# Performance work log

Hardware: AMD Instinct MI355X
Metric: run time of the kernel (lower is better)

## Reference

```python
import jax, jax.numpy as jnp
import numpy as np

DIM = 512
HEADS = 8
HEAD_DIM = DIM // HEADS
WINDOW = 128
TOKEN_SELF_ATTN_VALUE = -5e4  # lucidrains local-attention constant for shared_qk self mask


def setup_inputs() -> dict:
    key = jax.random.key(0)
    k1, k2, k3, k4 = jax.random.split(key, 4)
    B, N = 4, 8192
    x = jax.random.normal(k1, (B, N, DIM), dtype=jnp.float32)
    w_qkv = jax.random.normal(k2, (3 * DIM, DIM), dtype=jnp.float32) * (DIM ** -0.5)
    w_proj = jax.random.normal(k3, (DIM, DIM), dtype=jnp.float32) * (DIM ** -0.5)
    b_proj = jax.random.normal(k4, (DIM,), dtype=jnp.float32) * 0.01
    return {"x": x, "w_qkv": w_qkv, "w_proj": w_proj, "b_proj": b_proj}


def _look_around(b):
    # b: [B,H,nw,w,D] -> [B,H,nw,2w,D] = concat(prev_window, cur_window); window 0 padded with zeros
    padded = jnp.pad(b, ((0, 0), (0, 0), (1, 0), (0, 0), (0, 0)))
    return jnp.concatenate([padded[:, :, :-1], b], axis=3)


def _local_attn(q, k, v):
    # causal sliding-window attention, window=128, look_backward=1, shared_qk
    B, H, N, D = q.shape
    w = WINDOW
    nw = N // w
    scale = D ** -0.5
    # shared_qk: l2-normalize keys (F.normalize, eps=1e-12)
    k = k / jnp.clip(jnp.linalg.norm(k, axis=-1, keepdims=True), 1e-12, None)

    bq = q.reshape(B, H, nw, w, D)
    bk = _look_around(k.reshape(B, H, nw, w, D))  # [B,H,nw,2w,D]
    bv = _look_around(v.reshape(B, H, nw, w, D))

    t = jnp.arange(N).reshape(nw, w)
    t_pad = jnp.pad(t, ((1, 0), (0, 0)), constant_values=-1)
    bq_t = t                                         # [nw, w]
    bq_k = jnp.concatenate([t_pad[:-1], t], axis=1)  # [nw, 2w]

    sim = jnp.einsum('bhwie,bhwje->bhwij', bq, bk) * scale  # [B,H,nw,w,2w]

    self_mask = bq_t[:, :, None] == bq_k[:, None, :]
    causal_mask = bq_t[:, :, None] < bq_k[:, None, :]
    pad_mask = (bq_k == -1)[:, None, :]
    mask_value = -jnp.finfo(sim.dtype).max
    sim = jnp.where(self_mask, TOKEN_SELF_ATTN_VALUE, sim)
    sim = jnp.where(causal_mask | pad_mask, mask_value, sim)

    attn = jax.nn.softmax(sim, axis=-1)  # dropout is identity in eval mode
    out = jnp.einsum('bhwij,bhwje->bhwie', attn, bv)
    return out.reshape(B, H, N, D)


def reference(x, w_qkv, w_proj, b_proj):
    B, N, C = x.shape
    qkv = x @ w_qkv.T  # [B,N,3C]
    q, k, v = jnp.split(qkv, 3, axis=-1)
    to_heads = lambda t: t.reshape(B, N, HEADS, HEAD_DIM).transpose(0, 2, 1, 3)
    out = _local_attn(to_heads(q), to_heads(k), to_heads(v))  # [B,H,N,D]
    out = out.transpose(0, 2, 1, 3).reshape(B, N, C)
    return out @ w_proj.T + b_proj
```

## Files before the change

kernel.cpp:

```cpp
#include <hip/hip_runtime.h>
#include <stdint.h>

typedef uint16_t u16;
typedef __bf16 bf16x8 __attribute__((ext_vector_type(8)));
typedef float f32x4 __attribute__((ext_vector_type(4)));
typedef uint16_t u16x4 __attribute__((ext_vector_type(4)));
typedef uint16_t u16x8 __attribute__((ext_vector_type(8)));

typedef __attribute__((address_space(1))) void as1_void;
typedef __attribute__((address_space(3))) void as3_void;

__device__ __forceinline__ float bf2f(u16 b) {
    union { uint32_t u; float f; } v; v.u = ((uint32_t)b) << 16; return v.f;
}
__device__ __forceinline__ u16 f2bf(float f) {
    union { float f; uint32_t u; } v; v.f = f;
    uint32_t u = v.u;
    u += 0x7fffu + ((u >> 16) & 1u);
    return (u16)(u >> 16);
}
__device__ __forceinline__ void gload_lds16(const u16* g, u16* l) {
    __builtin_amdgcn_global_load_lds((as1_void*)g, (as3_void*)l, 16, 0, 0);
}

__global__ __launch_bounds__(256) void cvt3(
    const float* __restrict__ x,  u16* __restrict__ xb,
    const float* __restrict__ wq, u16* __restrict__ wqb,
    const float* __restrict__ wp, u16* __restrict__ wpb)
{
    const float* src; u16* dst; int base, nb;
    const int b = blockIdx.x;
    if (b < 1024)      { src = x;  dst = xb;  base = b;        nb = 1024; }
    else if (b < 1072) { src = wq; dst = wqb; base = b - 1024; nb = 48;   }
    else               { src = wp; dst = wpb; base = b - 1072; nb = 16;   }
    size_t i = ((size_t)base * 256 + threadIdx.x) * 8;
    const size_t stride = (size_t)nb * 256 * 8;
    #pragma unroll
    for (int it = 0; it < 8; ++it, i += stride) {
        f32x4 a = *(const f32x4*)(src + i);
        f32x4 c = *(const f32x4*)(src + i + 4);
        u16x8 o;
        o[0] = f2bf(a[0]); o[1] = f2bf(a[1]); o[2] = f2bf(a[2]); o[3] = f2bf(a[3]);
        o[4] = f2bf(c[0]); o[5] = f2bf(c[1]); o[6] = f2bf(c[2]); o[7] = f2bf(c[3]);
        *(u16x8*)(dst + i) = o;
    }
}

template<int NT, bool C_F32, bool NORMK, bool BIAS>
__global__ __launch_bounds__(512, 2) void gemm_pipe256(
    const u16* __restrict__ A, int lda,
    const u16* __restrict__ B, int ldb,
    const float* __restrict__ bias,
    void* __restrict__ Cv, int ldc)
{
    __shared__ u16 lA[4][256 * 32];
    __shared__ u16 lB[4][256 * 32];

    const int tid  = threadIdx.x;
    const int lane = tid & 63;
    const int wave = tid >> 6;
    const int wm = wave >> 2;
    const int wn = wave & 3;
    const int cl = lane & 15;
    const int gr = lane >> 4;

    int fid = blockIdx.y * gridDim.x + blockIdx.x;
    const int nwg = gridDim.x * gridDim.y;
    fid = (fid & 7) * (nwg >> 3) + (fid >> 3);
    const int row0 = (fid / gridDim.x) * 256;
    const int col0 = (fid % gridDim.x) * 256;

    f32x4 acc[8][4] = {};

    auto STAGE = [&](int t, int d) {
        const int k0 = t * 32;
        #pragma unroll
        for (int i = 0; i < 2; ++i) {
            const int id  = i * 512 + tid;
            const int row = id >> 2;
            const int sch = ((id & 3) - ((row >> 1) & 3)) & 3;
            gload_lds16(A + (size_t)(row0 + row) * lda + k0 + sch * 8, &lA[d][id * 8]);
            gload_lds16(B + (size_t)(col0 + row) * ldb + k0 + sch * 8, &lB[d][id * 8]);
        }
    };

    bf16x8 af[8], bfv[4];
    auto READ_A = [&](int t, int m) -> bf16x8 {
        const u16* la = lA[t & 3];
        const int ra = wm * 128 + m * 16 + cl;
        return *(const bf16x8*)&la[ra * 32 + ((gr + (ra >> 1)) & 3) * 8];
    };
    auto READ_B = [&](int t, int n) -> bf16x8 {
        const u16* lb = lB[t & 3];
        const int rb = wn * 64 + n * 16 + cl;
        return *(const bf16x8*)&lb[rb * 32 + ((gr + (rb >> 1)) & 3) * 8];
    };

    STAGE(0, 0); STAGE(1, 1); STAGE(2, 2);
    asm volatile("s_waitcnt vmcnt(4)" ::: "memory");
    __builtin_amdgcn_s_barrier();
    #pragma unroll
    for (int m = 0; m < 8; ++m) af[m] = READ_A(0, m);
    #pragma unroll
    for (int n = 0; n < 4; ++n) bfv[n] = READ_B(0, n);

    #pragma unroll
    for (int t = 0; t < NT; ++t) {
        if (t + 3 < NT) STAGE(t + 3, (t + 3) & 3);
        __builtin_amdgcn_s_setprio(1);
        #pragma unroll
        for (int m = 0; m < 8; ++m) {
            #pragma unroll
            for (int n = 0; n < 4; ++n)
                acc[m][n] = __builtin_amdgcn_mfma_f32_16x16x32_bf16(af[m], bfv[n], acc[m][n], 0, 0, 0);
            if (t + 1 < NT) af[m] = READ_A(t + 1, m);
        }
        __builtin_amdgcn_s_setprio(0);
        if (t + 1 < NT) {
            #pragma unroll
            for (int n = 0; n < 4; ++n) bfv[n] = READ_B(t + 1, n);
        }
        if (t < NT - 1) {
            asm volatile("s_waitcnt lgkmcnt(0)" ::: "memory");
            if (t + 3 < NT) asm volatile("s_waitcnt vmcnt(4)" ::: "memory");
            else            asm volatile("s_waitcnt vmcnt(0)" ::: "memory");
            __builtin_amdgcn_s_barrier();
        }
    }

    if constexpr (NORMK) {
        if (col0 + wn * 64 >= 512 && col0 + wn * 64 < 1024) {
            #pragma unroll
            for (int m = 0; m < 8; ++m)
                #pragma unroll
                for (int j = 0; j < 4; ++j) {
                    float ss = 0.f;
                    #pragma unroll
                    for (int n = 0; n < 4; ++n) ss += acc[m][n][j] * acc[m][n][j];
                    ss += __shfl_xor(ss, 1);
                    ss += __shfl_xor(ss, 2);
                    ss += __shfl_xor(ss, 4);
                    ss += __shfl_xor(ss, 8);
                    const float scl = 1.f / fmaxf(sqrtf(ss), 1e-12f);
                    #pragma unroll
                    for (int n = 0; n < 4; ++n) acc[m][n][j] *= scl;
                }
        }
    }

    #pragma unroll
    for (int m = 0; m < 8; ++m) {
        const int r = row0 + wm * 128 + m * 16 + gr * 4;
        #pragma unroll
        for (int n = 0; n < 4; ++n) {
            const int c = col0 + wn * 64 + n * 16 + cl;
            float bv = 0.f;
            if constexpr (BIAS) bv = bias[c];
            #pragma unroll
            for (int j = 0; j < 4; ++j) {
                const float val = acc[m][n][j] + bv;
                if constexpr (C_F32) ((float*)Cv)[(size_t)(r + j) * ldc + c] = val;
                else                 ((u16*)Cv)[(size_t)(r + j) * ldc + c] = f2bf(val);
            }
        }
    }
}

template<bool A_F32, bool C_F32, bool NORMK>
__global__ __launch_bounds__(256) void gemm_bt_f32(
    const void* __restrict__ Av, int lda,
    const float* __restrict__ B, int ldb,
    const float* __restrict__ bias,
    void* __restrict__ Cv, int ldc,
    int K)
{
    __shared__ u16 lA[128 * 32];
    __shared__ u16 lB[128 * 32];

    const int tid  = threadIdx.x;
    const int lane = tid & 63;
    const int wave = tid >> 6;
    const int wr   = (wave >> 1) * 64;
    const int wc   = (wave & 1) * 64;
    const int row0 = blockIdx.y * 128;
    const int col0 = blockIdx.x * 128;

    f32x4 acc[4][4] = {};

    for (int k0 = 0; k0 < K; k0 += 32) {
        #pragma unroll
        for (int i = 0; i < 4; ++i) {
            const int idx = i * 256 + tid;
            const int r = idx >> 3;
            const int p = (idx & 7) * 4;
            u16x4 a4, b4;
            if constexpr (A_F32) {
                const float* Af = (const float*)Av;
                f32x4 va = *(const f32x4*)(Af + (size_t)(row0 + r) * lda + k0 + p);
                a4[0] = f2bf(va[0]); a4[1] = f2bf(va[1]); a4[2] = f2bf(va[2]); a4[3] = f2bf(va[3]);
            } else {
                const u16* Ab = (const u16*)Av;
                a4 = *(const u16x4*)(Ab + (size_t)(row0 + r) * lda + k0 + p);
            }
            {
                f32x4 vb = *(const f32x4*)(B + (size_t)(col0 + r) * ldb + k0 + p);
                b4[0] = f2bf(vb[0]); b4[1] = f2bf(vb[1]); b4[2] = f2bf(vb[2]); b4[3] = f2bf(vb[3]);
            }
            *(u16x4*)&lA[r * 32 + p] = a4;
            *(u16x4*)&lB[r * 32 + p] = b4;
        }
        __syncthreads();

        bf16x8 af[4], bfv[4];
        #pragma unroll
        for (int m = 0; m < 4; ++m)
            af[m] = *(const bf16x8*)(lA + (wr + m * 16 + (lane & 15)) * 32 + (lane >> 4) * 8);
        #pragma unroll
        for (int n = 0; n < 4; ++n)
            bfv[n] = *(const bf16x8*)(lB + (wc + n * 16 + (lane & 15)) * 32 + (lane >> 4) * 8);
        #pragma unroll
        for (int m = 0; m < 4; ++m)
            #pragma unroll
            for (int n = 0; n < 4; ++n)
                acc[m][n] = __builtin_amdgcn_mfma_f32_16x16x32_bf16(af[m], bfv[n], acc[m][n], 0, 0, 0);
        __syncthreads();
    }

    if constexpr (NORMK) {
        if (col0 >= 512 && col0 < 1024) {
            #pragma unroll
            for (int m = 0; m < 4; ++m)
                #pragma unroll
                for (int j = 0; j < 4; ++j) {
                    float ss = 0.f;
                    #pragma unroll
                    for (int n = 0; n < 4; ++n) ss += acc[m][n][j] * acc[m][n][j];
                    ss += __shfl_xor(ss, 1);
                    ss += __shfl_xor(ss, 2);
                    ss += __shfl_xor(ss, 4);
                    ss += __shfl_xor(ss, 8);
                    const float scl = 1.f / fmaxf(sqrtf(ss), 1e-12f);
                    #pragma unroll
                    for (int n = 0; n < 4; ++n) acc[m][n][j] *= scl;
                }
        }
    }

    #pragma unroll
    for (int m = 0; m < 4; ++m) {
        const int r = row0 + wr + m * 16 + ((lane >> 4) << 2);
        #pragma unroll
        for (int n = 0; n < 4; ++n) {
            const int c = col0 + wc + n * 16 + (lane & 15);
            const float bv = bias ? bias[c] : 0.f;
            #pragma unroll
            for (int j = 0; j < 4; ++j) {
                const float val = acc[m][n][j] + bv;
                if constexpr (C_F32) ((float*)Cv)[(size_t)(r + j) * ldc + c] = val;
                else                 ((u16*)Cv)[(size_t)(r + j) * ldc + c] = f2bf(val);
            }
        }
    }
}

__global__ __launch_bounds__(512, 4) void attn_kernel(const u16* qkv, u16* o)
{
    constexpr int CC = 1536;
    constexpr int NTOK = 8192;
    constexpr int KP = 72;
    constexpr int VP = 136;
    constexpr int PP = 136;
    __shared__ u16 kn[128 * KP];
    __shared__ u16 vT[64 * VP];
    __shared__ u16 Pl[128 * PP];

    const int tid  = threadIdx.x;
    const int lane = tid & 63;
    const int wave = tid >> 6;
    const int cl = lane & 15;
    const int gr = lane >> 4;

    int blk = blockIdx.x;
    blk = (blk & 7) * (gridDim.x >> 3) + (blk >> 3);

    const int iw  = blk & 63;
    const int h   = (blk >> 6) & 7;
    const int b   = blk >> 9;

    const int tq0 = iw * 128;
    const int tkc0 = tq0 - 128;
    const int tkc1 = tq0;
    const size_t rowbase = (size_t)b * NTOK;
    const u16* qbase = qkv + rowbase * CC + h * 64;
    const u16* kbase = qbase + 512;
    const u16* vbase = qbase + 1024;

    const int wrow = wave * 16;
    bf16x8 qf[2];
    #pragma unroll
    for (int kk = 0; kk < 2; ++kk)
        qf[kk] = *(const bf16x8*)(qbase + (size_t)(tq0 + wrow + cl) * CC + kk * 32 + gr * 8);

    f32x4 oacc[4] = {};
    float m_run[4] = {-3.0e38f, -3.0e38f, -3.0e38f, -3.0e38f};
    float l_run[4] = {0.f, 0.f, 0.f, 0.f};

    auto CHUNK = [&](int tkc) {
        f32x4 s[8] = {};
        #pragma unroll
        for (int n = 0; n < 8; ++n)
            #pragma unroll
            for (int kk = 0; kk < 2; ++kk) {
                const bf16x8 kf = *(const bf16x8*)&kn[(n * 16 + cl) * KP + kk * 32 + gr * 8];
                s[n] = __builtin_amdgcn_mfma_f32_16x16x32_bf16(qf[kk], kf, s[n], 0, 0, 0);
            }
        float pmax[4] = {-3.0e38f, -3.0e38f, -3.0e38f, -3.0e38f};
        #pragma unroll
        for (int n = 0; n < 8; ++n) {
            const int tkk = tkc + n * 16 + cl;
            const bool pad = tkk < 0;
            #pragma unroll
            for (int j = 0; j < 4; ++j) {
                const int tq = tq0 + wrow + gr * 4 + j;
                float sv = s[n][j] * 0.125f;
                const int rel = tkk - tq;
                sv = (rel == 0) ? -5.0e4f : sv;
                sv = (rel > 0 || pad) ? -6.0e4f : sv;
                s[n][j] = sv;
                pmax[j] = fmaxf(pmax[j], sv);
            }
        }
        float cold[4];
        #pragma unroll
        for (int j = 0; j < 4; ++j) {
            pmax[j] = fmaxf(pmax[j], __shfl_xor(pmax[j], 1));
            pmax[j] = fmaxf(pmax[j], __shfl_xor(pmax[j], 2));
            pmax[j] = fmaxf(pmax[j], __shfl_xor(pmax[j], 4));
            pmax[j] = fmaxf(pmax[j], __shfl_xor(pmax[j], 8));
            const float mn = fmaxf(m_run[j], pmax[j]);
            cold[j] = __expf(m_run[j] - mn);
            m_run[j] = mn;
            l_run[j] *= cold[j];
        }
        #pragma unroll
        for (int n = 0; n < 8; ++n)
            #pragma unroll
            for (int j = 0; j < 4; ++j) {
                const float p = __expf(s[n][j] - m_run[j]);
                s[n][j] = p;
                l_run[j] += p;
            }
        #pragma unroll
        for (int n = 0; n < 4; ++n) {
            f32x4 t = oacc[n];
            t[0] *= cold[0]; t[1] *= cold[1]; t[2] *= cold[2]; t[3] *= cold[3];
            oacc[n] = t;
        }
        #pragma unroll
        for (int n = 0; n < 8; ++n)
            #pragma unroll
            for (int j = 0; j < 4; ++j)
                Pl[(wrow + gr * 4 + j) * PP + n * 16 + cl] = f2bf(s[n][j]);
        __syncthreads();
        #pragma unroll
        for (int kk = 0; kk < 4; ++kk) {
            const bf16x8 pa = *(const bf16x8*)&Pl[(wrow + cl) * PP + kk * 32 + gr * 8];
            #pragma unroll
            for (int n = 0; n < 4; ++n) {
                const bf16x8 vb = *(const bf16x8*)&vT[(n * 16 + cl) * VP + kk * 32 + gr * 8];
                oacc[n] = __builtin_amdgcn_mfma_f32_16x16x32_bf16(pa, vb, oacc[n], 0, 0, 0);
            }
        }
    };

    #pragma unroll
    for (int p = 0; p < 2; ++p) {
        const int id = tid + p * 512;
        const int row = id >> 3, dc = id & 7;
        u16x8 v8 = {};
        if (tkc0 >= 0) v8 = *(const u16x8*)(kbase + (size_t)(tkc0 + row) * CC + dc * 8);
        *(u16x8*)&kn[row * KP + dc * 8] = v8;
    }
    #pragma unroll
    for (int p = 0; p < 2; ++p) {
        const int id = tid + p * 512;
        const int key = id & 127, dc = id >> 7;
        u16x8 v8 = {};
        if (tkc0 >= 0) v8 = *(const u16x8*)(vbase + (size_t)(tkc0 + key) * CC + dc * 8);
        #pragma unroll
        for (int e = 0; e < 8; ++e) vT[(dc * 8 + e) * VP + key] = v8[e];
    }
    u16x8 kr[2], vr[2];
    #pragma unroll
    for (int p = 0; p < 2; ++p) {
        const int id = tid + p * 512;
        kr[p] = *(const u16x8*)(kbase + (size_t)(tkc1 + (id >> 3)) * CC + (id & 7) * 8);
        vr[p] = *(const u16x8*)(vbase + (size_t)(tkc1 + (id & 127)) * CC + (id >> 7) * 8);
    }
    __syncthreads();

    CHUNK(tkc0);
    __syncthreads();

    #pragma unroll
    for (int p = 0; p < 2; ++p) {
        const int id = tid + p * 512;
        *(u16x8*)&kn[(id >> 3) * KP + (id & 7) * 8] = kr[p];
    }
    #pragma unroll
    for (int p = 0; p < 2; ++p) {
        const int id = tid + p * 512;
        const int key = id & 127, dc = id >> 7;
        #pragma unroll
        for (int e = 0; e < 8; ++e) vT[(dc * 8 + e) * VP + key] = vr[p][e];
    }
    __syncthreads();

    CHUNK(tkc1);

    float inv[4];
    #pragma unroll
    for (int j = 0; j < 4; ++j) {
        l_run[j] += __shfl_xor(l_run[j], 1);
        l_run[j] += __shfl_xor(l_run[j], 2);
        l_run[j] += __shfl_xor(l_run[j], 4);
        l_run[j] += __shfl_xor(l_run[j], 8);
        inv[j] = 1.f / l_run[j];
    }
    u16* obase = o + rowbase * CC + h * 64;
    const int r0 = tq0 + wrow + gr * 4;
    #pragma unroll
    for (int n = 0; n < 4; ++n) {
        const int d = n * 16 + cl;
        #pragma unroll
        for (int j = 0; j < 4; ++j)
            obase[(size_t)(r0 + j) * CC + d] = f2bf(oacc[n][j] * inv[j]);
    }
}

extern "C" void kernel_launch(void* const* d_in, const int* in_sizes, int n_in,
                              void* d_out, int out_size, void* d_ws, size_t ws_size,
                              hipStream_t stream)
{
    (void)in_sizes; (void)n_in; (void)out_size;
    const float* x      = (const float*)d_in[0];
    const float* w_qkv  = (const float*)d_in[1];
    const float* w_proj = (const float*)d_in[2];
    const float* b_proj = (const float*)d_in[3];
    float* out = (float*)d_out;

    const int BN = 4 * 8192;
    const size_t qkv_b = (size_t)BN * 1536 * 2;
    const size_t xb_b  = (size_t)BN * 512 * 2;
    const size_t wq_b  = (size_t)1536 * 512 * 2;
    const size_t wp_b  = (size_t)512 * 512 * 2;

    uint8_t* p = (uint8_t*)d_ws;
    u16* qkv = (u16*)p;

    if (ws_size >= qkv_b + xb_b + wq_b + wp_b) {
        u16* xb  = (u16*)(p + qkv_b);
        u16* wqb = (u16*)(p + qkv_b + xb_b);
        u16* wpb = (u16*)(p + qkv_b + xb_b + wq_b);
        cvt3<<<1088, 256, 0, stream>>>(x, xb, w_qkv, wqb, w_proj, wpb);
        gemm_pipe256<16, false, true, false><<<dim3(6, 128), 512, 0, stream>>>(
            xb, 512, wqb, 512, nullptr, qkv, 1536);
        attn_kernel<<<dim3(4 * 8 * 64), 512, 0, stream>>>(qkv, qkv);
        gemm_pipe256<16, true, false, true><<<dim3(2, 128), 512, 0, stream>>>(
            qkv, 1536, wpb, 512, b_proj, out, 512);
    } else {
        gemm_bt_f32<true, false, true><<<dim3(12, BN / 128), 256, 0, stream>>>(
            x, 512, w_qkv, 512, nullptr, qkv, 1536, 512);
        attn_kernel<<<dim3(4 * 8 * 64), 512, 0, stream>>>(qkv, qkv);
        gemm_bt_f32<false, true, false><<<dim3(4, BN / 128), 256, 0, stream>>>(
            qkv, 1536, w_proj, 512, b_proj, out, 512, 512);
    }
}
```

Measured before the change: 166.6 us.

## Fuse fp32-to-bf16 conversion of x into the QKV GEMM load path

Removes the separate conversion pass that turned x into a bf16 copy in workspace. The QKV GEMM now loads fp32 x tiles straight into LDS and converts to bf16 when reading fragments. The M tile shrinks to 128 rows so the larger fp32 tile fits in LDS. This cuts a full read and write of the 32M-element activation, at the cost of twice the global and LDS traffic for A inside the GEMM and extra conversion instructions in the inner loop.

```diff
diff --git a/kernel.cpp b/kernel.cpp
--- a/kernel.cpp
+++ b/kernel.cpp
@@ -23,26 +23,147 @@
     __builtin_amdgcn_global_load_lds((as1_void*)g, (as3_void*)l, 16, 0, 0);
 }
 
-__global__ __launch_bounds__(256) void cvt3(
-    const float* __restrict__ x,  u16* __restrict__ xb,
+__global__ __launch_bounds__(256) void cvt_w(
     const float* __restrict__ wq, u16* __restrict__ wqb,
     const float* __restrict__ wp, u16* __restrict__ wpb)
 {
-    const float* src; u16* dst; int base, nb;
+    const float* src; u16* dst; int base;
     const int b = blockIdx.x;
-    if (b < 1024)      { src = x;  dst = xb;  base = b;        nb = 1024; }
-    else if (b < 1072) { src = wq; dst = wqb; base = b - 1024; nb = 48;   }
-    else               { src = wp; dst = wpb; base = b - 1072; nb = 16;   }
-    size_t i = ((size_t)base * 256 + threadIdx.x) * 8;
-    const size_t stride = (size_t)nb * 256 * 8;
-    #pragma unroll
-    for (int it = 0; it < 8; ++it, i += stride) {
-        f32x4 a = *(const f32x4*)(src + i);
-        f32x4 c = *(const f32x4*)(src + i + 4);
-        u16x8 o;
-        o[0] = f2bf(a[0]); o[1] = f2bf(a[1]); o[2] = f2bf(a[2]); o[3] = f2bf(a[3]);
-        o[4] = f2bf(c[0]); o[5] = f2bf(c[1]); o[6] = f2bf(c[2]); o[7] = f2bf(c[3]);
-        *(u16x8*)(dst + i) = o;
+    if (b < 384) { src = wq; dst = wqb; base = b; }
+    else         { src = wp; dst = wpb; base = b - 384; }
+    const size_t i = ((size_t)base * 256 + threadIdx.x) * 8;
+    f32x4 a = *(const f32x4*)(src + i);
+    f32x4 c = *(const f32x4*)(src + i + 4);
+    u16x8 o;
+    o[0] = f2bf(a[0]); o[1] = f2bf(a[1]); o[2] = f2bf(a[2]); o[3] = f2bf(a[3]);
+    o[4] = f2bf(c[0]); o[5] = f2bf(c[1]); o[6] = f2bf(c[2]); o[7] = f2bf(c[3]);
+    *(u16x8*)(dst + i) = o;
+}
+
+template<int NT, bool NORMK>
+__global__ __launch_bounds__(512, 2) void gemm_fx(
+    const float* __restrict__ A, int lda,
+    const u16* __restrict__ B, int ldb,
+    u16* __restrict__ C, int ldc)
+{
+    __shared__ float lA[4][128 * 32];
+    __shared__ u16   lB[4][256 * 32];
+
+    const int tid  = threadIdx.x;
+    const int lane = tid & 63;
+    const int wave = tid >> 6;
+    const int wm = wave >> 2;
+    const int wn = wave & 3;
+    const int cl = lane & 15;
+    const int gr = lane >> 4;
+
+    int fid = blockIdx.y * gridDim.x + blockIdx.x;
+    const int nwg = gridDim.x * gridDim.y;
+    fid = (fid & 7) * (nwg >> 3) + (fid >> 3);
+    const int row0 = (fid / gridDim.x) * 128;
+    const int col0 = (fid % gridDim.x) * 256;
+
+    f32x4 acc[4][4] = {};
+
+    auto STAGE = [&](int t, int d) {
+        const int k0 = t * 32;
+        #pragma unroll
+        for (int i = 0; i < 2; ++i) {
+            const int id = i * 512 + tid;
+            const int rowa = id >> 3;
+            const int scha = ((id & 7) - (rowa & 7)) & 7;
+            gload_lds16((const u16*)(A + (size_t)(row0 + rowa) * lda + k0 + scha * 4),
+                        (u16*)&lA[d][id * 4]);
+            const int rowb = id >> 2;
+            const int schb = ((id & 3) - ((rowb >> 1) & 3)) & 3;
+            gload_lds16(B + (size_t)(col0 + rowb) * ldb + k0 + schb * 8,
+                        &lB[d][id * 8]);
+        }
+    };
+
+    bf16x8 af[4], bfv[4];
+    auto READ_A = [&](int t, int m) -> bf16x8 {
+        const float* la = lA[t & 3];
+        const int ra = wm * 64 + m * 16 + cl;
+        const int s0 = (gr * 2 + ra) & 7;
+        const int s1 = (gr * 2 + 1 + ra) & 7;
+        const f32x4 x0 = *(const f32x4*)&la[ra * 32 + s0 * 4];
+        const f32x4 x1 = *(const f32x4*)&la[ra * 32 + s1 * 4];
+        bf16x8 t8;
+        t8[0] = (__bf16)x0[0]; t8[1] = (__bf16)x0[1];
+        t8[2] = (__bf16)x0[2]; t8[3] = (__bf16)x0[3];
+        t8[4] = (__bf16)x1[0]; t8[5] = (__bf16)x1[1];
+        t8[6] = (__bf16)x1[2]; t8[7] = (__bf16)x1[3];
+        return t8;
+    };
+    auto READ_B = [&](int t, int n) -> bf16x8 {
+        const u16* lb = lB[t & 3];
+        const int rb = wn * 64 + n * 16 + cl;
+        return *(const bf16x8*)&lb[rb * 32 + ((gr + (rb >> 1)) & 3) * 8];
+    };
+
+    STAGE(0, 0); STAGE(1, 1); STAGE(2, 2);
+    asm volatile("s_waitcnt vmcnt(4)" ::: "memory");
+    __builtin_amdgcn_s_barrier();
+    #pragma unroll
+    for (int m = 0; m < 4; ++m) af[m] = READ_A(0, m);
+    #pragma unroll
+    for (int n = 0; n < 4; ++n) bfv[n] = READ_B(0, n);
+
+    #pragma unroll
+    for (int t = 0; t < NT; ++t) {
+        if (t + 3 < NT) STAGE(t + 3, (t + 3) & 3);
+        __builtin_amdgcn_s_setprio(1);
+        #pragma unroll
+        for (int m = 0; m < 4; ++m) {
+            #pragma unroll
+            for (int n = 0; n < 4; ++n)
+                acc[m][n] = __builtin_amdgcn_mfma_f32_16x16x32_bf16(af[m], bfv[n], acc[m][n], 0, 0, 0);
+            if (t + 1 < NT) af[m] = READ_A(t + 1, m);
+        }
+        __builtin_amdgcn_s_setprio(0);
+        if (t + 1 < NT) {
+            #pragma unroll
+            for (int n = 0; n < 4; ++n) bfv[n] = READ_B(t + 1, n);
+        }
+        if (t < NT - 1) {
+            asm volatile("s_waitcnt lgkmcnt(0)" ::: "memory");
+            if (t + 3 < NT) asm volatile("s_waitcnt vmcnt(4)" ::: "memory");
+            else            asm volatile("s_waitcnt vmcnt(0)" ::: "memory");
+            __builtin_amdgcn_s_barrier();
+        }
+    }
+
+    if constexpr (NORMK) {
+        if (col0 + wn * 64 >= 512 && col0 + wn * 64 < 1024) {
+            #pragma unroll
+            for (int m = 0; m < 4; ++m)
+                #pragma unroll
+                for (int j = 0; j < 4; ++j) {
+                    float ss = 0.f;
+                    #pragma unroll
+                    for (int n = 0; n < 4; ++n) ss += acc[m][n][j] * acc[m][n][j];
+                    ss += __shfl_xor(ss, 1);
+                    ss += __shfl_xor(ss, 2);
+                    ss += __shfl_xor(ss, 4);
+                    ss += __shfl_xor(ss, 8);
+                    const float scl = 1.f / fmaxf(sqrtf(ss), 1e-12f);
+                    #pragma unroll
+                    for (int n = 0; n < 4; ++n) acc[m][n][j] *= scl;
+                }
+        }
+    }
+
+    #pragma unroll
+    for (int m = 0; m < 4; ++m) {
+        const int r = row0 + wm * 64 + m * 16 + gr * 4;
+        #pragma unroll
+        for (int n = 0; n < 4; ++n) {
+            const int c = col0 + wn * 64 + n * 16 + cl;
+            #pragma unroll
+            for (int j = 0; j < 4; ++j)
+                C[(size_t)(r + j) * ldc + c] = f2bf(acc[m][n][j]);
+        }
     }
 }
 
@@ -451,20 +572,18 @@
 
     const int BN = 4 * 8192;
     const size_t qkv_b = (size_t)BN * 1536 * 2;
-    const size_t xb_b  = (size_t)BN * 512 * 2;
     const size_t wq_b  = (size_t)1536 * 512 * 2;
     const size_t wp_b  = (size_t)512 * 512 * 2;
 
     uint8_t* p = (uint8_t*)d_ws;
     u16* qkv = (u16*)p;
 
-    if (ws_size >= qkv_b + xb_b + wq_b + wp_b) {
-        u16* xb  = (u16*)(p + qkv_b);
-        u16* wqb = (u16*)(p + qkv_b + xb_b);
-        u16* wpb = (u16*)(p + qkv_b + xb_b + wq_b);
-        cvt3<<<1088, 256, 0, stream>>>(x, xb, w_qkv, wqb, w_proj, wpb);
-        gemm_pipe256<16, false, true, false><<<dim3(6, 128), 512, 0, stream>>>(
-            xb, 512, wqb, 512, nullptr, qkv, 1536);
+    if (ws_size >= qkv_b + wq_b + wp_b) {
+        u16* wqb = (u16*)(p + qkv_b);
+        u16* wpb = (u16*)(p + qkv_b + wq_b);
+        cvt_w<<<512, 256, 0, stream>>>(w_qkv, wqb, w_proj, wpb);
+        gemm_fx<16, true><<<dim3(6, 256), 512, 0, stream>>>(
+            x, 512, wqb, 512, qkv, 1536);
         attn_kernel<<<dim3(4 * 8 * 64), 512, 0, stream>>>(qkv, qkv);
         gemm_pipe256<16, true, false, true><<<dim3(2, 128), 512, 0, stream>>>(
             qkv, 1536, wpb, 512, b_proj, out, 512);
```

Measured after the change: 168.2 us. Within noise of the previous version (+0.9%).
